# Performance work log

Measured on AMD Instinct MI355X. Metric: run time of the kernel, lower is better.

## Reference

```python
import jax, jax.numpy as jnp
import numpy as np

BATCH, INPUT_SIZE, STEPS = 256, 512, 256
HIDDEN = 512


def setup_inputs() -> dict:
    key = jax.random.key(0)
    ks = jax.random.split(key, 5)
    s = 1.0 / np.sqrt(HIDDEN)
    return {
        "x": jax.random.normal(ks[0], (BATCH, INPUT_SIZE, STEPS), dtype=jnp.float32),
        "weight_ih": jax.random.uniform(ks[1], (3 * HIDDEN, INPUT_SIZE), jnp.float32, -s, s),
        "weight_hh": jax.random.uniform(ks[2], (3 * HIDDEN, HIDDEN), jnp.float32, -s, s),
        "bias_ih": jax.random.uniform(ks[3], (3 * HIDDEN,), jnp.float32, -s, s),
        "bias_hh": jax.random.uniform(ks[4], (3 * HIDDEN,), jnp.float32, -s, s),
    }


def reference(x, weight_ih, weight_hh, bias_ih, bias_hh):
    # x: [B, input_size, steps]; run a GRUCell over the time axis, return final hidden.
    B = x.shape[0]
    # Precompute all input projections in one big GEMM: [steps, B, 3H]
    gi_all = jnp.einsum('bis,gi->sbg', x, weight_ih) + bias_ih

    def step(h, gi):
        gh = h @ weight_hh.T + bias_hh  # [B, 3H]
        i_r, i_z, i_n = jnp.split(gi, 3, axis=-1)
        h_r, h_z, h_n = jnp.split(gh, 3, axis=-1)
        r = jax.nn.sigmoid(i_r + h_r)
        z = jax.nn.sigmoid(i_z + h_z)
        n = jnp.tanh(i_n + r * h_n)
        h_new = (1.0 - z) * n + z * h
        return h_new, None

    h0 = jnp.zeros((B, HIDDEN), dtype=x.dtype)
    h_final, _ = jax.lax.scan(step, h0, gi_all)
    return h_final
```

## Files before the change

kernel.cpp:

```cpp
#include <hip/hip_runtime.h>
#include <stdint.h>

typedef __attribute__((ext_vector_type(8))) short bf16x8;
typedef __attribute__((ext_vector_type(4))) short s16x4;
typedef __attribute__((ext_vector_type(4))) float f32x4;
typedef __attribute__((ext_vector_type(4))) unsigned u32x4;

#define AS1 __attribute__((address_space(1)))
#define AS3 __attribute__((address_space(3)))

static __device__ __forceinline__ void gload_lds16(const void* g, void* l) {
  __builtin_amdgcn_global_load_lds((const AS1 unsigned int*)g,
                                   (AS3 unsigned int*)l, 16, 0, 0);
}

static __device__ __forceinline__ short f2bs(float f) {
  unsigned u = __builtin_bit_cast(unsigned, f);
  unsigned r = (u + 0x7fffu + ((u >> 16) & 1u)) >> 16;
  return (short)r;
}
static __device__ __forceinline__ float bs2f(short s) {
  unsigned u = ((unsigned)(unsigned short)s) << 16;
  return __builtin_bit_cast(float, u);
}

static __device__ __forceinline__ float sigmoid_f(float x) {
  return 1.0f / (1.0f + __expf(-x));
}
static __device__ __forceinline__ float tanh_f(float x) {
  float ax = fabsf(x);
  float e  = __expf(-2.0f * ax);
  float t  = (1.0f - e) / (1.0f + e);
  return copysignf(t, x);
}

#define BATCH 256
#define HID   512
#define STEPS 256
#define G3    1536

__global__ __launch_bounds__(256) void convert_kernel(const float* __restrict__ src,
                                                      short* __restrict__ dst, int n4) {
  int i = blockIdx.x * 256 + threadIdx.x;
  if (i < n4) {
    float4 v = *(const float4*)(src + (size_t)i * 4);
    s16x4 o;
    o[0] = f2bs(v.x); o[1] = f2bs(v.y); o[2] = f2bs(v.z); o[3] = f2bs(v.w);
    *(s16x4*)(dst + (size_t)i * 4) = o;
  }
}

__global__ __launch_bounds__(256) void transpose_kernel(const float* __restrict__ x,
                                                        short* __restrict__ xT) {
  int bx = blockIdx.x;
  int st = bx & 7, it = (bx >> 3) & 15, b = bx >> 7;
  int s0 = st * 32, i0 = it * 32;
  int tid = threadIdx.x;
  __shared__ float tile[32][33];
  int il = tid >> 3, s4 = (tid & 7) * 4;
  float4 v = *(const float4*)(x + (size_t)b * 131072 + (size_t)(i0 + il) * 256 + s0 + s4);
  tile[il][s4 + 0] = v.x; tile[il][s4 + 1] = v.y;
  tile[il][s4 + 2] = v.z; tile[il][s4 + 3] = v.w;
  __syncthreads();
  int sl = tid >> 3, iv = (tid & 7) * 4;
  s16x4 o;
  o[0] = f2bs(tile[iv + 0][sl]); o[1] = f2bs(tile[iv + 1][sl]);
  o[2] = f2bs(tile[iv + 2][sl]); o[3] = f2bs(tile[iv + 3][sl]);
  *(s16x4*)(xT + (size_t)(s0 + sl) * 131072 + (size_t)b * 512 + i0 + iv) = o;
}

__global__ __launch_bounds__(256) void phase1_kernel(const short* __restrict__ A,
                                                     const short* __restrict__ B,
                                                     const float* __restrict__ bias,
                                                     short* __restrict__ out, int M) {
  int MT = M >> 7;
  int bx = blockIdx.x;
  int mt = bx % MT, nt = bx / MT;
  int m0 = mt * 128, n0 = nt * 128;
  int tid = threadIdx.x, w = tid >> 6, lane = tid & 63;
  int lm = lane & 15, q = lane >> 4;
  int wm = w & 1, wn = w >> 1;
  __shared__ short As[128 * 32];
  __shared__ short Bs[128 * 32];
  f32x4 acc[4][4] = {};
  int srow = lane >> 2;
  int scol = (lane & 3) * 8;

  for (int kt = 0; kt < 16; ++kt) {
#pragma unroll
    for (int i2 = 0; i2 < 2; ++i2) {
      int i = w * 2 + i2;
      int row = i * 16 + srow;
      gload_lds16(A + (size_t)(m0 + row) * 512 + kt * 32 + scol, As + i * 512);
      gload_lds16(B + (size_t)(n0 + row) * 512 + kt * 32 + scol, Bs + i * 512);
    }
    __syncthreads();
    bf16x8 av[4], bv[4];
#pragma unroll
    for (int f = 0; f < 4; ++f) {
      av[f] = *(const bf16x8*)(As + (wm * 64 + f * 16 + lm) * 32 + q * 8);
      bv[f] = *(const bf16x8*)(Bs + (wn * 64 + f * 16 + lm) * 32 + q * 8);
    }
#pragma unroll
    for (int fm = 0; fm < 4; ++fm)
#pragma unroll
      for (int fn = 0; fn < 4; ++fn)
        acc[fm][fn] = __builtin_amdgcn_mfma_f32_16x16x32_bf16(av[fm], bv[fn], acc[fm][fn], 0, 0, 0);
    __syncthreads();
  }
#pragma unroll
  for (int fn = 0; fn < 4; ++fn) {
    int g = n0 + wn * 64 + fn * 16 + lm;
    float bi = bias[g];
#pragma unroll
    for (int fm = 0; fm < 4; ++fm) {
      int rb = m0 + wm * 64 + fm * 16 + q * 4;
#pragma unroll
      for (int r = 0; r < 4; ++r)
        out[(size_t)(rb + r) * G3 + g] = f2bs(acc[fm][fn][r] + bi);
    }
  }
}

__global__ __launch_bounds__(256) void scan_kernel(const short* __restrict__ gi,
                                                   const short* __restrict__ Whh,
                                                   const float* __restrict__ bias_hh,
                                                   unsigned* __restrict__ hbuf,
                                                   float* __restrict__ hmaster,
                                                   int CH, int step_base, int first) {
  int bid = blockIdx.x;
  int xcd = bid & 7, slot = bid >> 3;
  int group = xcd + 8 * (slot >> 4);
  int j = slot & 15;
  int tid = threadIdx.x;
  int w = tid >> 6, lane = tid & 63;
  int lm = lane & 15, q = lane >> 4;
  int grow = group * 16;

  __shared__ short h_lds[16 * 520];
  __shared__ float gh_lds[16][100];
  __shared__ float h_loc[512];
  __shared__ float bhh[96];

  bf16x8 Bf[2][16];
  if (w < 3) {
#pragma unroll
    for (int tau = 0; tau < 2; ++tau)
#pragma unroll
      for (int kt = 0; kt < 16; ++kt) {
        int row = w * 512 + j * 32 + tau * 16 + lm;
        Bf[tau][kt] = *(const bf16x8*)(Whh + (size_t)row * 512 + kt * 32 + q * 8);
      }
  }

  if (tid < 96) {
    int p = tid >> 5, cc = tid & 31;
    bhh[tid] = bias_hh[p * 512 + j * 32 + cc];
  }
#pragma unroll
  for (int u = 0; u < 2; ++u) {
    int idx = tid + u * 256;
    int r = idx >> 5, cc = idx & 31;
    h_loc[idx] = first ? 0.0f : hmaster[(size_t)(grow + r) * 512 + j * 32 + cc];
  }
  __syncthreads();

  int i0 = tid, i1 = tid + 256;
  const short* gp0 = gi + (size_t)(grow + (i0 >> 5)) * G3 + j * 32 + (i0 & 31);
  const short* gp1 = gi + (size_t)(grow + (i1 >> 5)) * G3 + j * 32 + (i1 & 31);
  const size_t gstride = (size_t)256 * G3;

  short pg0r = gp0[0], pg0z = gp0[512], pg0n = gp0[1024];
  short pg1r = gp1[0], pg1z = gp1[512], pg1n = gp1[1024];

  unsigned o0 = (unsigned)tid * 16u;
  const int r0 = tid >> 7;
  const int colb = (tid & 127) * 4;
  short* lp = h_lds + r0 * 520 + colb;
  unsigned* grp_base = hbuf + (size_t)group * 8192;

  for (int t = 0; t < CH; ++t) {
    int gstep = step_base + t;
    int p = gstep & 1;
    const unsigned* src = grp_base + (size_t)p * 131072;
    unsigned want = (unsigned)gstep;

    u32x4 v0, v1, v2, v3, v4, v5, v6, v7;
    int spin = 0;
    for (;;) {
      asm volatile(
          "global_load_dwordx4 %0, %8, %16 sc0 sc1\n\t"
          "global_load_dwordx4 %1, %9, %16 sc0 sc1\n\t"
          "global_load_dwordx4 %2, %10, %16 sc0 sc1\n\t"
          "global_load_dwordx4 %3, %11, %16 sc0 sc1\n\t"
          "global_load_dwordx4 %4, %12, %16 sc0 sc1\n\t"
          "global_load_dwordx4 %5, %13, %16 sc0 sc1\n\t"
          "global_load_dwordx4 %6, %14, %16 sc0 sc1\n\t"
          "global_load_dwordx4 %7, %15, %16 sc0 sc1\n\t"
          "s_waitcnt vmcnt(0)"
          : "=&v"(v0), "=&v"(v1), "=&v"(v2), "=&v"(v3),
            "=&v"(v4), "=&v"(v5), "=&v"(v6), "=&v"(v7)
          : "v"(o0), "v"(o0 + 4096u), "v"(o0 + 8192u), "v"(o0 + 12288u),
            "v"(o0 + 16384u), "v"(o0 + 20480u), "v"(o0 + 24576u), "v"(o0 + 28672u),
            "s"(src)
          : "memory");
      unsigned d;
      d  = (v0[0] ^ want) | (v0[1] ^ want) | (v0[2] ^ want) | (v0[3] ^ want);
      d |= (v1[0] ^ want) | (v1[1] ^ want) | (v1[2] ^ want) | (v1[3] ^ want);
      d |= (v2[0] ^ want) | (v2[1] ^ want) | (v2[2] ^ want) | (v2[3] ^ want);
      d |= (v3[0] ^ want) | (v3[1] ^ want) | (v3[2] ^ want) | (v3[3] ^ want);
      d |= (v4[0] ^ want) | (v4[1] ^ want) | (v4[2] ^ want) | (v4[3] ^ want);
      d |= (v5[0] ^ want) | (v5[1] ^ want) | (v5[2] ^ want) | (v5[3] ^ want);
      d |= (v6[0] ^ want) | (v6[1] ^ want) | (v6[2] ^ want) | (v6[3] ^ want);
      d |= (v7[0] ^ want) | (v7[1] ^ want) | (v7[2] ^ want) | (v7[3] ^ want);
      if (((d & 0xffffu) == 0u) || (++spin > (1 << 16))) break;
      __builtin_amdgcn_s_sleep(1);
    }

#define STASH(vv, c)                                                         \
    {                                                                        \
      s16x4 o_;                                                              \
      o_[0] = (short)(vv[0] >> 16); o_[1] = (short)(vv[1] >> 16);            \
      o_[2] = (short)(vv[2] >> 16); o_[3] = (short)(vv[3] >> 16);            \
      *(s16x4*)(lp + (c) * 1040) = o_;                                       \
    }
    STASH(v0, 0) STASH(v1, 1) STASH(v2, 2) STASH(v3, 3)
    STASH(v4, 4) STASH(v5, 5) STASH(v6, 6) STASH(v7, 7)
#undef STASH

    float cg0r = bs2f(pg0r), cg0z = bs2f(pg0z), cg0n = bs2f(pg0n);
    float cg1r = bs2f(pg1r), cg1z = bs2f(pg1z), cg1n = bs2f(pg1n);
    {
      size_t o = (size_t)((t + 1 < CH) ? (t + 1) : t) * gstride;
      pg0r = gp0[o]; pg0z = gp0[o + 512]; pg0n = gp0[o + 1024];
      pg1r = gp1[o]; pg1z = gp1[o + 512]; pg1n = gp1[o + 1024];
    }
    asm volatile("s_waitcnt lgkmcnt(0)\n\ts_barrier" ::: "memory");
    __builtin_amdgcn_sched_barrier(0);

    if (w < 3) {
      f32x4 a0 = {0.f,0.f,0.f,0.f}, a1 = {0.f,0.f,0.f,0.f};
      f32x4 a2 = {0.f,0.f,0.f,0.f}, a3 = {0.f,0.f,0.f,0.f};
#pragma unroll
      for (int kt = 0; kt < 8; ++kt) {
        bf16x8 a = *(const bf16x8*)(h_lds + lm * 520 + kt * 32 + q * 8);
        a0 = __builtin_amdgcn_mfma_f32_16x16x32_bf16(a, Bf[0][kt], a0, 0, 0, 0);
        a1 = __builtin_amdgcn_mfma_f32_16x16x32_bf16(a, Bf[1][kt], a1, 0, 0, 0);
      }
#pragma unroll
      for (int kt = 8; kt < 16; ++kt) {
        bf16x8 a = *(const bf16x8*)(h_lds + lm * 520 + kt * 32 + q * 8);
        a2 = __builtin_amdgcn_mfma_f32_16x16x32_bf16(a, Bf[0][kt], a2, 0, 0, 0);
        a3 = __builtin_amdgcn_mfma_f32_16x16x32_bf16(a, Bf[1][kt], a3, 0, 0, 0);
      }
#pragma unroll
      for (int r = 0; r < 4; ++r) {
        gh_lds[q * 4 + r][w * 32 + lm]      = a0[r] + a2[r];
        gh_lds[q * 4 + r][w * 32 + 16 + lm] = a1[r] + a3[r];
      }
    }
    asm volatile("s_waitcnt lgkmcnt(0)\n\ts_barrier" ::: "memory");
    __builtin_amdgcn_sched_barrier(0);

    unsigned tagp = (unsigned)(gstep + 1);
    unsigned* dstb = grp_base + (size_t)(1 - p) * 131072;
    {
      int r = i0 >> 5, cc = i0 & 31;
      float hr = gh_lds[r][cc]      + bhh[cc];
      float hz = gh_lds[r][32 + cc] + bhh[32 + cc];
      float hn = gh_lds[r][64 + cc] + bhh[64 + cc];
      float rr = sigmoid_f(cg0r + hr);
      float zz = sigmoid_f(cg0z + hz);
      float nn = tanh_f(cg0n + rr * hn);
      float hv = (1.0f - zz) * nn + zz * h_loc[i0];
      h_loc[i0] = hv;
      unsigned val = (((unsigned)(unsigned short)f2bs(hv)) << 16) | tagp;
      unsigned* dp = dstb + r * 512 + j * 32 + cc;
      asm volatile("global_store_dword %0, %1, off sc0 sc1" :: "v"(dp), "v"(val) : "memory");
    }
    {
      int r = i1 >> 5, cc = i1 & 31;
      float hr = gh_lds[r][cc]      + bhh[cc];
      float hz = gh_lds[r][32 + cc] + bhh[32 + cc];
      float hn = gh_lds[r][64 + cc] + bhh[64 + cc];
      float rr = sigmoid_f(cg1r + hr);
      float zz = sigmoid_f(cg1z + hz);
      float nn = tanh_f(cg1n + rr * hn);
      float hv = (1.0f - zz) * nn + zz * h_loc[i1];
      h_loc[i1] = hv;
      unsigned val = (((unsigned)(unsigned short)f2bs(hv)) << 16) | tagp;
      unsigned* dp = dstb + r * 512 + j * 32 + cc;
      asm volatile("global_store_dword %0, %1, off sc0 sc1" :: "v"(dp), "v"(val) : "memory");
    }
  }

#pragma unroll
  for (int u = 0; u < 2; ++u) {
    int idx = tid + u * 256;
    int r = idx >> 5, cc = idx & 31;
    hmaster[(size_t)(grow + r) * 512 + j * 32 + cc] = h_loc[idx];
  }
}

extern "C" void kernel_launch(void* const* d_in, const int* in_sizes, int n_in,
                              void* d_out, int out_size, void* d_ws, size_t ws_size,
                              hipStream_t stream) {
  const float* x   = (const float*)d_in[0];
  const float* Wih = (const float*)d_in[1];
  const float* Whh = (const float*)d_in[2];
  const float* bih = (const float*)d_in[3];
  const float* bhh = (const float*)d_in[4];
  float* out = (float*)d_out;
  char* ws = (char*)d_ws;

  const size_t XT_BYTES   = (size_t)256 * 256 * 512 * 2;
  const size_t W_BYTES    = (size_t)1536 * 512 * 2;
  const size_t HBUF_BYTES = (size_t)2 * 256 * 512 * 4;
  const size_t FIXED = XT_BYTES + 2 * W_BYTES + HBUF_BYTES + 4096;

  int CH = 256;
  while (CH > 4 && FIXED + (size_t)CH * 256 * G3 * 2 > ws_size) CH >>= 1;

  size_t off = 0;
  short* gi = (short*)(ws + off);          off += (size_t)CH * 256 * G3 * 2;
  short* xT = (short*)(ws + off);          off += XT_BYTES;
  short* WihB = (short*)(ws + off);        off += W_BYTES;
  short* WhhB = (short*)(ws + off);        off += W_BYTES;
  unsigned* hbuf = (unsigned*)(ws + off);

  hipMemsetAsync(hbuf, 0, HBUF_BYTES, stream);

  convert_kernel<<<768, 256, 0, stream>>>(Wih, WihB, 196608);
  convert_kernel<<<768, 256, 0, stream>>>(Whh, WhhB, 196608);
  transpose_kernel<<<32768, 256, 0, stream>>>(x, xT);

  int nch = 256 / CH;
  for (int c = 0; c < nch; ++c) {
    int M = CH * 256;
    phase1_kernel<<<(M / 128) * 12, 256, 0, stream>>>(
        xT + (size_t)c * CH * 256 * 512, WihB, bih, gi, M);
    scan_kernel<<<256, 256, 0, stream>>>(gi, WhhB, bhh, hbuf, out,
                                         CH, c * CH, c == 0 ? 1 : 0);
  }
}
```

Measured before the change: 881.5 us.

## Fuse input-projection GEMM into persistent scan kernel with pipelined x staging

Removes the separate phase1 GEMM kernel and the gi workspace. Each scan block now keeps its W_ih slice in registers and computes the input projection for step t+1 while waiting for step t's hidden state. x tiles for t+2 are prefetched asynchronously into double-buffered, swizzled LDS. This drops the large gi write and read-back and one kernel launch, but doubles register pressure for weight fragments and puts extra MFMA work on the recurrent critical path of each step.

```diff
diff --git a/kernel.cpp b/kernel.cpp
--- a/kernel.cpp
+++ b/kernel.cpp
@@ -69,65 +69,14 @@
   *(s16x4*)(xT + (size_t)(s0 + sl) * 131072 + (size_t)b * 512 + i0 + iv) = o;
 }
 
-__global__ __launch_bounds__(256) void phase1_kernel(const short* __restrict__ A,
-                                                     const short* __restrict__ B,
-                                                     const float* __restrict__ bias,
-                                                     short* __restrict__ out, int M) {
-  int MT = M >> 7;
-  int bx = blockIdx.x;
-  int mt = bx % MT, nt = bx / MT;
-  int m0 = mt * 128, n0 = nt * 128;
-  int tid = threadIdx.x, w = tid >> 6, lane = tid & 63;
-  int lm = lane & 15, q = lane >> 4;
-  int wm = w & 1, wn = w >> 1;
-  __shared__ short As[128 * 32];
-  __shared__ short Bs[128 * 32];
-  f32x4 acc[4][4] = {};
-  int srow = lane >> 2;
-  int scol = (lane & 3) * 8;
-
-  for (int kt = 0; kt < 16; ++kt) {
-#pragma unroll
-    for (int i2 = 0; i2 < 2; ++i2) {
-      int i = w * 2 + i2;
-      int row = i * 16 + srow;
-      gload_lds16(A + (size_t)(m0 + row) * 512 + kt * 32 + scol, As + i * 512);
-      gload_lds16(B + (size_t)(n0 + row) * 512 + kt * 32 + scol, Bs + i * 512);
-    }
-    __syncthreads();
-    bf16x8 av[4], bv[4];
-#pragma unroll
-    for (int f = 0; f < 4; ++f) {
-      av[f] = *(const bf16x8*)(As + (wm * 64 + f * 16 + lm) * 32 + q * 8);
-      bv[f] = *(const bf16x8*)(Bs + (wn * 64 + f * 16 + lm) * 32 + q * 8);
-    }
-#pragma unroll
-    for (int fm = 0; fm < 4; ++fm)
-#pragma unroll
-      for (int fn = 0; fn < 4; ++fn)
-        acc[fm][fn] = __builtin_amdgcn_mfma_f32_16x16x32_bf16(av[fm], bv[fn], acc[fm][fn], 0, 0, 0);
-    __syncthreads();
-  }
-#pragma unroll
-  for (int fn = 0; fn < 4; ++fn) {
-    int g = n0 + wn * 64 + fn * 16 + lm;
-    float bi = bias[g];
-#pragma unroll
-    for (int fm = 0; fm < 4; ++fm) {
-      int rb = m0 + wm * 64 + fm * 16 + q * 4;
-#pragma unroll
-      for (int r = 0; r < 4; ++r)
-        out[(size_t)(rb + r) * G3 + g] = f2bs(acc[fm][fn][r] + bi);
-    }
-  }
-}
-
-__global__ __launch_bounds__(256) void scan_kernel(const short* __restrict__ gi,
-                                                   const short* __restrict__ Whh,
-                                                   const float* __restrict__ bias_hh,
-                                                   unsigned* __restrict__ hbuf,
-                                                   float* __restrict__ hmaster,
-                                                   int CH, int step_base, int first) {
+__global__ __launch_bounds__(256, 1) void scan_kernel(const short* __restrict__ xT,
+                                                      const short* __restrict__ Wih,
+                                                      const short* __restrict__ Whh,
+                                                      const float* __restrict__ bias_ih,
+                                                      const float* __restrict__ bias_hh,
+                                                      unsigned* __restrict__ hbuf,
+                                                      float* __restrict__ hmaster) {
+  const int CH = 256;
   int bid = blockIdx.x;
   int xcd = bid & 7, slot = bid >> 3;
   int group = xcd + 8 * (slot >> 4);
@@ -137,12 +86,15 @@
   int lm = lane & 15, q = lane >> 4;
   int grow = group * 16;
 
-  __shared__ short h_lds[16 * 520];
+  __shared__ __align__(16) short h_lds[16 * 520];
+  __shared__ __align__(16) short x_lds[2][8192];
   __shared__ float gh_lds[16][100];
+  __shared__ float gi_lds[2][16][100];
   __shared__ float h_loc[512];
-  __shared__ float bhh[96];
+  __shared__ float bih_s[96], bhh_s[96];
 
   bf16x8 Bf[2][16];
+  bf16x8 Wf[2][16];
   if (w < 3) {
 #pragma unroll
     for (int tau = 0; tau < 2; ++tau)
@@ -150,28 +102,63 @@
       for (int kt = 0; kt < 16; ++kt) {
         int row = w * 512 + j * 32 + tau * 16 + lm;
         Bf[tau][kt] = *(const bf16x8*)(Whh + (size_t)row * 512 + kt * 32 + q * 8);
+        Wf[tau][kt] = *(const bf16x8*)(Wih + (size_t)row * 512 + kt * 32 + q * 8);
       }
   }
-
   if (tid < 96) {
-    int p = tid >> 5, cc = tid & 31;
-    bhh[tid] = bias_hh[p * 512 + j * 32 + cc];
-  }
-#pragma unroll
-  for (int u = 0; u < 2; ++u) {
-    int idx = tid + u * 256;
-    int r = idx >> 5, cc = idx & 31;
-    h_loc[idx] = first ? 0.0f : hmaster[(size_t)(grow + r) * 512 + j * 32 + cc];
-  }
+    int g = (tid >> 5) * 512 + j * 32 + (tid & 31);
+    bih_s[tid] = bias_ih[g];
+    bhh_s[tid] = bias_hh[g];
+  }
+  h_loc[tid] = 0.0f;
+  h_loc[tid + 256] = 0.0f;
+
+  int xr[4], xc[4];
+#pragma unroll
+  for (int c = 0; c < 4; ++c) {
+    int rr_ = c * 4 + w;
+    xr[c] = rr_;
+    xc[c] = ((lane * 16) ^ ((rr_ & 7) << 4)) >> 1;
+  }
+
+#define XSTAGE(s, par) do {                                                  \
+    const short* xsb = xT + (size_t)(s) * 131072;                            \
+    _Pragma("unroll")                                                        \
+    for (int c = 0; c < 4; ++c)                                              \
+      gload_lds16(xsb + (size_t)(grow + xr[c]) * 512 + xc[c],                \
+                  &x_lds[par][c * 2048 + tid * 8]);                          \
+  } while (0)
+
+#define XGEMM(pn) do {                                                       \
+    f32x4 a0 = {0.f,0.f,0.f,0.f}, a1 = {0.f,0.f,0.f,0.f};                    \
+    f32x4 a2 = {0.f,0.f,0.f,0.f}, a3 = {0.f,0.f,0.f,0.f};                    \
+    _Pragma("unroll")                                                        \
+    for (int kt = 0; kt < 8; ++kt) {                                         \
+      bf16x8 a = *(const bf16x8*)(&x_lds[pn][lm * 512 +                      \
+                      ((kt * 32 + q * 8) ^ ((lm & 7) << 3))]);               \
+      a0 = __builtin_amdgcn_mfma_f32_16x16x32_bf16(a, Wf[0][kt], a0, 0, 0, 0); \
+      a1 = __builtin_amdgcn_mfma_f32_16x16x32_bf16(a, Wf[1][kt], a1, 0, 0, 0); \
+    }                                                                        \
+    _Pragma("unroll")                                                        \
+    for (int kt = 8; kt < 16; ++kt) {                                        \
+      bf16x8 a = *(const bf16x8*)(&x_lds[pn][lm * 512 +                      \
+                      ((kt * 32 + q * 8) ^ ((lm & 7) << 3))]);               \
+      a2 = __builtin_amdgcn_mfma_f32_16x16x32_bf16(a, Wf[0][kt], a2, 0, 0, 0); \
+      a3 = __builtin_amdgcn_mfma_f32_16x16x32_bf16(a, Wf[1][kt], a3, 0, 0, 0); \
+    }                                                                        \
+    _Pragma("unroll")                                                        \
+    for (int r = 0; r < 4; ++r) {                                            \
+      gi_lds[pn][q * 4 + r][w * 32 + lm]      = a0[r] + a2[r];               \
+      gi_lds[pn][q * 4 + r][w * 32 + 16 + lm] = a1[r] + a3[r];               \
+    }                                                                        \
+  } while (0)
+
+  XSTAGE(0, 0);
+  XSTAGE(1, 1);
+  asm volatile("s_waitcnt vmcnt(0)" ::: "memory");
   __syncthreads();
-
-  int i0 = tid, i1 = tid + 256;
-  const short* gp0 = gi + (size_t)(grow + (i0 >> 5)) * G3 + j * 32 + (i0 & 31);
-  const short* gp1 = gi + (size_t)(grow + (i1 >> 5)) * G3 + j * 32 + (i1 & 31);
-  const size_t gstride = (size_t)256 * G3;
-
-  short pg0r = gp0[0], pg0z = gp0[512], pg0n = gp0[1024];
-  short pg1r = gp1[0], pg1z = gp1[512], pg1n = gp1[1024];
+  if (w < 3) XGEMM(0);
+  __syncthreads();
 
   unsigned o0 = (unsigned)tid * 16u;
   const int r0 = tid >> 7;
@@ -180,10 +167,18 @@
   unsigned* grp_base = hbuf + (size_t)group * 8192;
 
   for (int t = 0; t < CH; ++t) {
-    int gstep = step_base + t;
-    int p = gstep & 1;
+    int p = t & 1;
     const unsigned* src = grp_base + (size_t)p * 131072;
-    unsigned want = (unsigned)gstep;
+    unsigned want = (unsigned)t;
+
+    asm volatile("s_waitcnt lgkmcnt(0)\n\ts_barrier" ::: "memory");
+    __builtin_amdgcn_sched_barrier(0);
+
+    {
+      int s = (t + 2 < CH) ? (t + 2) : (CH - 1);
+      XSTAGE(s, p);
+    }
+    if (w < 3 && t + 1 < CH) XGEMM((t + 1) & 1);
 
     u32x4 v0, v1, v2, v3, v4, v5, v6, v7;
     int spin = 0;
@@ -228,13 +223,6 @@
     STASH(v4, 4) STASH(v5, 5) STASH(v6, 6) STASH(v7, 7)
 #undef STASH
 
-    float cg0r = bs2f(pg0r), cg0z = bs2f(pg0z), cg0n = bs2f(pg0n);
-    float cg1r = bs2f(pg1r), cg1z = bs2f(pg1z), cg1n = bs2f(pg1n);
-    {
-      size_t o = (size_t)((t + 1 < CH) ? (t + 1) : t) * gstride;
-      pg0r = gp0[o]; pg0z = gp0[o + 512]; pg0n = gp0[o + 1024];
-      pg1r = gp1[o]; pg1z = gp1[o + 512]; pg1n = gp1[o + 1024];
-    }
     asm volatile("s_waitcnt lgkmcnt(0)\n\ts_barrier" ::: "memory");
     __builtin_amdgcn_sched_barrier(0);
 
@@ -262,16 +250,20 @@
     asm volatile("s_waitcnt lgkmcnt(0)\n\ts_barrier" ::: "memory");
     __builtin_amdgcn_sched_barrier(0);
 
-    unsigned tagp = (unsigned)(gstep + 1);
+    unsigned tagp = (unsigned)(t + 1);
     unsigned* dstb = grp_base + (size_t)(1 - p) * 131072;
     {
+      int i0 = tid;
       int r = i0 >> 5, cc = i0 & 31;
-      float hr = gh_lds[r][cc]      + bhh[cc];
-      float hz = gh_lds[r][32 + cc] + bhh[32 + cc];
-      float hn = gh_lds[r][64 + cc] + bhh[64 + cc];
-      float rr = sigmoid_f(cg0r + hr);
-      float zz = sigmoid_f(cg0z + hz);
-      float nn = tanh_f(cg0n + rr * hn);
+      float cgr = gi_lds[p][r][cc]      + bih_s[cc];
+      float cgz = gi_lds[p][r][32 + cc] + bih_s[32 + cc];
+      float cgn = gi_lds[p][r][64 + cc] + bih_s[64 + cc];
+      float hr = gh_lds[r][cc]      + bhh_s[cc];
+      float hz = gh_lds[r][32 + cc] + bhh_s[32 + cc];
+      float hn = gh_lds[r][64 + cc] + bhh_s[64 + cc];
+      float rr = sigmoid_f(cgr + hr);
+      float zz = sigmoid_f(cgz + hz);
+      float nn = tanh_f(cgn + rr * hn);
       float hv = (1.0f - zz) * nn + zz * h_loc[i0];
       h_loc[i0] = hv;
       unsigned val = (((unsigned)(unsigned short)f2bs(hv)) << 16) | tagp;
@@ -279,13 +271,17 @@
       asm volatile("global_store_dword %0, %1, off sc0 sc1" :: "v"(dp), "v"(val) : "memory");
     }
     {
+      int i1 = tid + 256;
       int r = i1 >> 5, cc = i1 & 31;
-      float hr = gh_lds[r][cc]      + bhh[cc];
-      float hz = gh_lds[r][32 + cc] + bhh[32 + cc];
-      float hn = gh_lds[r][64 + cc] + bhh[64 + cc];
-      float rr = sigmoid_f(cg1r + hr);
-      float zz = sigmoid_f(cg1z + hz);
-      float nn = tanh_f(cg1n + rr * hn);
+      float cgr = gi_lds[p][r][cc]      + bih_s[cc];
+      float cgz = gi_lds[p][r][32 + cc] + bih_s[32 + cc];
+      float cgn = gi_lds[p][r][64 + cc] + bih_s[64 + cc];
+      float hr = gh_lds[r][cc]      + bhh_s[cc];
+      float hz = gh_lds[r][32 + cc] + bhh_s[32 + cc];
+      float hn = gh_lds[r][64 + cc] + bhh_s[64 + cc];
+      float rr = sigmoid_f(cgr + hr);
+      float zz = sigmoid_f(cgz + hz);
+      float nn = tanh_f(cgn + rr * hn);
       float hv = (1.0f - zz) * nn + zz * h_loc[i1];
       h_loc[i1] = hv;
       unsigned val = (((unsigned)(unsigned short)f2bs(hv)) << 16) | tagp;
@@ -293,6 +289,10 @@
       asm volatile("global_store_dword %0, %1, off sc0 sc1" :: "v"(dp), "v"(val) : "memory");
     }
   }
+#undef XSTAGE
+#undef XGEMM
+
+  asm volatile("s_waitcnt vmcnt(0)" ::: "memory");
 
 #pragma unroll
   for (int u = 0; u < 2; ++u) {
@@ -316,13 +316,8 @@
   const size_t XT_BYTES   = (size_t)256 * 256 * 512 * 2;
   const size_t W_BYTES    = (size_t)1536 * 512 * 2;
   const size_t HBUF_BYTES = (size_t)2 * 256 * 512 * 4;
-  const size_t FIXED = XT_BYTES + 2 * W_BYTES + HBUF_BYTES + 4096;
-
-  int CH = 256;
-  while (CH > 4 && FIXED + (size_t)CH * 256 * G3 * 2 > ws_size) CH >>= 1;
 
   size_t off = 0;
-  short* gi = (short*)(ws + off);          off += (size_t)CH * 256 * G3 * 2;
   short* xT = (short*)(ws + off);          off += XT_BYTES;
   short* WihB = (short*)(ws + off);        off += W_BYTES;
   short* WhhB = (short*)(ws + off);        off += W_BYTES;
@@ -334,12 +329,5 @@
   convert_kernel<<<768, 256, 0, stream>>>(Whh, WhhB, 196608);
   transpose_kernel<<<32768, 256, 0, stream>>>(x, xT);
 
-  int nch = 256 / CH;
-  for (int c = 0; c < nch; ++c) {
-    int M = CH * 256;
-    phase1_kernel<<<(M / 128) * 12, 256, 0, stream>>>(
-        xT + (size_t)c * CH * 256 * 512, WihB, bih, gi, M);
-    scan_kernel<<<256, 256, 0, stream>>>(gi, WhhB, bhh, hbuf, out,
-                                         CH, c * CH, c == 0 ? 1 : 0);
-  }
-}
+  scan_kernel<<<256, 256, 0, stream>>>(xT, WihB, WhhB, bih, bhh, hbuf, out);
+}
```

Result: slower. 945.6 us (+7.3%).
